# Kernel tuning notes

Measured on AMD Instinct MI355X. Metric: run time of the kernel, lower is better.

## Reference

```python
import jax, jax.numpy as jnp
import numpy as np

N_NODES = 50000
N_EDGES = 600000
NODE_DIM = 128
BOND_DIM = 16
HIDDEN = 128
DEPTH = 3


def setup_inputs() -> dict:
    key = jax.random.key(0)
    ks = jax.random.split(key, 10)
    rng = np.random.default_rng(0)
    half = N_EDGES // 2
    u = rng.integers(0, N_NODES, size=half)
    v = rng.integers(0, N_NODES, size=half)
    # forward edges followed by their reverses so rev_edge_index is well-defined
    edge_index = np.stack([np.concatenate([u, v]), np.concatenate([v, u])]).astype(np.int32)
    rev_edge_index = np.concatenate([np.arange(half, 2 * half), np.arange(0, half)]).astype(np.int32)

    def lin(k, fan_in, fan_out):
        kw, kb = jax.random.split(k)
        s = 1.0 / np.sqrt(fan_in)
        W = jax.random.uniform(kw, (fan_in, fan_out), jnp.float32, -s, s)
        b = jax.random.uniform(kb, (fan_out,), jnp.float32, -s, s)
        return W, b

    Wi, bi = lin(ks[0], NODE_DIM + BOND_DIM, HIDDEN)
    Wh, bh = lin(ks[1], HIDDEN, HIDDEN)
    Wo, bo = lin(ks[2], NODE_DIM + HIDDEN, HIDDEN)
    x = jax.random.normal(ks[3], (N_NODES, NODE_DIM), jnp.float32)
    edge_attr = jax.random.normal(ks[4], (N_EDGES, BOND_DIM), jnp.float32)
    return {
        "x": x,
        "edge_attr": edge_attr,
        "Wi": Wi, "bi": bi,
        "Wh": Wh, "bh": bh,
        "Wo": Wo, "bo": bo,
        "edge_index": jnp.asarray(edge_index),
        "rev_edge_index": jnp.asarray(rev_edge_index),
    }


def reference(x, edge_attr, Wi, bi, Wh, bh, Wo, bo, edge_index, rev_edge_index):
    # BondMessagePassing.forward (depth=3, dropout in eval mode = identity)
    src, dst = edge_index[0], edge_index[1]
    N = x.shape[0]
    # H_0 = relu(W_i([x[src] ; edge_attr]))  -> [E, H]
    H0 = jax.nn.relu(jnp.concatenate([x[src], edge_attr], axis=1) @ Wi + bi)
    H = H0
    for _ in range(DEPTH - 1):
        # aggregate incoming edge messages per node, then gather back to edges
        agg = jax.ops.segment_sum(H, dst, num_segments=N)  # [N, H]
        M = agg[src] - H[rev_edge_index]                   # subtract reverse-edge message
        H = jax.nn.relu(H0 + M @ Wh + bh)
    M = jax.ops.segment_sum(H, dst, num_segments=N)        # [N, H]
    # nodes with no incoming message fall back to their input features
    M = jnp.where(jnp.sum(M, axis=1, keepdims=True) == 0, x, M)
    return jax.nn.relu(jnp.concatenate([x, M], axis=1) @ Wo + bo)
```

## Files before the change

### kernel.cpp

```cpp
#include <hip/hip_runtime.h>
#include <hip/hip_bf16.h>

#define E_EDGES 600000
#define N_NODES 50000

typedef __attribute__((ext_vector_type(8))) short bf16x8;
typedef __attribute__((ext_vector_type(4))) short s16x4;
typedef __attribute__((ext_vector_type(4))) float f32x4;
typedef unsigned short u16;

static __device__ __forceinline__ float bf2f(u16 u) {
    unsigned int x = ((unsigned int)u) << 16;
    return __builtin_bit_cast(float, x);
}
static __device__ __forceinline__ u16 f2bf(float f) {
    return __builtin_bit_cast(u16, __float2bfloat16(f));
}
static __device__ __forceinline__ int xcd_swz(int orig, int nwg) {
    int q = nwg >> 3, r = nwg & 7;
    int x = orig & 7, o = orig >> 3;
    int base = (x < r) ? x * (q + 1) : r * (q + 1) + (x - r) * q;
    return base + o;
}

__global__ __launch_bounds__(256) void zero_kernel(f32x4* __restrict__ p, int n4) {
    int i = blockIdx.x * 256 + threadIdx.x;
    if (i < n4) p[i] = f32x4{0.f, 0.f, 0.f, 0.f};
}
__global__ __launch_bounds__(256) void zero_int_kernel(int* __restrict__ p, int n) {
    int i = blockIdx.x * 256 + threadIdx.x;
    if (i < n) p[i] = 0;
}

__global__ void prep_kernel(const float* __restrict__ Wi, const float* __restrict__ Wh,
                            const float* __restrict__ Wo,
                            short* __restrict__ WiT, short* __restrict__ WhT,
                            short* __restrict__ WoT) {
    int idx = blockIdx.x * 256 + threadIdx.x;
    if (idx < 128 * 160) {
        int j = idx / 160, k = idx % 160;
        WiT[idx] = (k < 144) ? (short)f2bf(Wi[k * 128 + j]) : (short)0;
    } else if (idx < 128 * 160 + 128 * 128) {
        int t = idx - 128 * 160;
        int j = t / 128, k = t % 128;
        WhT[t] = (short)f2bf(Wh[k * 128 + j]);
    } else if (idx < 128 * 160 + 128 * 128 + 128 * 256) {
        int t = idx - 128 * 160 - 128 * 128;
        int j = t / 256, k = t % 256;
        WoT[t] = (short)f2bf(Wo[k * 128 + j]);
    }
}

__global__ __launch_bounds__(256) void prepx_kernel(const float* __restrict__ x,
                                                    const float* __restrict__ ea,
                                                    short* __restrict__ xb,
                                                    short* __restrict__ eb) {
    const int NX4 = N_NODES * 128 / 4;
    const int NE4 = E_EDGES * 16 / 4;
    int i = blockIdx.x * 256 + threadIdx.x;
    if (i < NX4) {
        f32x4 v = ((const f32x4*)x)[i];
        s16x4 o;
#pragma unroll
        for (int j = 0; j < 4; ++j) o[j] = (short)f2bf(v[j]);
        ((s16x4*)xb)[i] = o;
    } else if (i < NX4 + NE4) {
        int t = i - NX4;
        f32x4 v = ((const f32x4*)ea)[t];
        s16x4 o;
#pragma unroll
        for (int j = 0; j < 4; ++j) o[j] = (short)f2bf(v[j]);
        ((s16x4*)eb)[t] = o;
    }
}

__global__ __launch_bounds__(256) void count_kernel(const int* __restrict__ ei,
                                                    int* __restrict__ deg) {
    int e = blockIdx.x * 256 + threadIdx.x;
    if (e < E_EDGES) atomicAdd(&deg[ei[E_EDGES + e]], 1);
}

__global__ __launch_bounds__(1024) void scan_kernel(const int* __restrict__ deg,
                                                    int* __restrict__ offs) {
    __shared__ int wsum[16];
    __shared__ int carry;
    const int t = threadIdx.x, lane = t & 63, wv = t >> 6;
    if (t == 0) { carry = 0; offs[0] = 0; }
    __syncthreads();
    for (int base = 0; base < N_NODES; base += 1024) {
        int i = base + t;
        int v = (i < N_NODES) ? deg[i] : 0;
        int s = v;
#pragma unroll
        for (int o = 1; o < 64; o <<= 1) {
            int u = __shfl_up(s, o, 64);
            if (lane >= o) s += u;
        }
        if (lane == 63) wsum[wv] = s;
        __syncthreads();
        if (wv == 0 && lane < 16) {
            int ws = wsum[lane];
#pragma unroll
            for (int o = 1; o < 16; o <<= 1) {
                int u = __shfl_up(ws, o, 16);
                if (lane >= o) ws += u;
            }
            wsum[lane] = ws;
        }
        __syncthreads();
        int wpre = (wv > 0) ? wsum[wv - 1] : 0;
        int incl = carry + wpre + s;
        if (i < N_NODES) offs[i + 1] = incl;
        __syncthreads();
        if (t == 1023) carry = incl;
        __syncthreads();
    }
}

__global__ __launch_bounds__(256) void scatter_kernel(const int* __restrict__ ei,
                                                      int* __restrict__ offs,
                                                      int* __restrict__ eids) {
    int e = blockIdx.x * 256 + threadIdx.x;
    if (e < E_EDGES) {
        int d = ei[E_EDGES + e];
        int p = atomicAdd(&offs[d], 1);
        eids[p] = e;
    }
}

__global__ __launch_bounds__(256) void segsum_kernel(const short* __restrict__ H,
                                                     const int* __restrict__ eids,
                                                     const int* __restrict__ offs,
                                                     float* __restrict__ agg,
                                                     float* __restrict__ flg) {
    const int w = threadIdx.x >> 6, l = threadIdx.x & 63;
    const int n = blockIdx.x * 4 + w;
    if (n >= N_NODES) return;
    int b = (n == 0) ? 0 : offs[n - 1];
    int en = offs[n];
    float s0 = 0.f, s1 = 0.f, t0 = 0.f, t1 = 0.f;
    int j = b;
    for (; j + 2 <= en; j += 2) {
        int e0 = eids[j], e1 = eids[j + 1];
        unsigned int pk0 = *(const unsigned int*)(H + (size_t)e0 * 128 + l * 2);
        unsigned int pk1 = *(const unsigned int*)(H + (size_t)e1 * 128 + l * 2);
        s0 += bf2f((u16)(pk0 & 0xffffu));
        s1 += bf2f((u16)(pk0 >> 16));
        t0 += bf2f((u16)(pk1 & 0xffffu));
        t1 += bf2f((u16)(pk1 >> 16));
    }
    if (j < en) {
        int e0 = eids[j];
        unsigned int pk0 = *(const unsigned int*)(H + (size_t)e0 * 128 + l * 2);
        s0 += bf2f((u16)(pk0 & 0xffffu));
        s1 += bf2f((u16)(pk0 >> 16));
    }
    s0 += t0; s1 += t1;
    agg[(size_t)n * 128 + l * 2] = s0;
    agg[(size_t)n * 128 + l * 2 + 1] = s1;
    if (flg) {
        float s = s0 + s1;
#pragma unroll
        for (int off = 32; off; off >>= 1) s += __shfl_xor(s, off, 64);
        if (l == 0) flg[n] = s;
    }
}

__global__ __launch_bounds__(256) void flag_kernel(const float* __restrict__ agg,
                                                   float* __restrict__ flg) {
    const int w = threadIdx.x >> 6, l = threadIdx.x & 63;
    const int n = blockIdx.x * 4 + w;
    if (n >= N_NODES) return;
    const float* r = agg + (size_t)n * 128 + l * 2;
    float s = r[0] + r[1];
#pragma unroll
    for (int off = 32; off; off >>= 1) s += __shfl_xor(s, off, 64);
    if (l == 0) flg[n] = s;
}

__global__ __launch_bounds__(256) void h0dst_kernel(
    const short* __restrict__ xb, const short* __restrict__ eb,
    const short* __restrict__ WiT, const float* __restrict__ bi,
    const int* __restrict__ ei, const int* __restrict__ eids,
    const int* __restrict__ offs, short* __restrict__ H0,
    float* __restrict__ agg1) {
    __shared__ short Bx[128 * 128];
    __shared__ short T[64 * 128];
    __shared__ int eloc[64], dstv[64];
    const int P = xcd_swz(blockIdx.x, gridDim.x) * 64;
    for (int i = threadIdx.x; i < 128 * 16; i += 256) {
        int row = i >> 4, cc = i & 15;
        int dstByte = row * 256 + ((cc * 16) ^ ((row & 7) << 4));
        *(bf16x8*)((char*)Bx + dstByte) = *(const bf16x8*)&WiT[row * 160 + cc * 8];
    }
    if (threadIdx.x < 64) {
        int e = eids[P + threadIdx.x];
        eloc[threadIdx.x] = e;
        dstv[threadIdx.x] = ei[E_EDGES + e];
    }
    __syncthreads();
    const int w = threadIdx.x >> 6, l = threadIdx.x & 63;
    const int c = l & 15, g = l >> 4;
    const int em = eloc[w * 16 + c];
    const int src_e = ei[em];
    const short* xr = xb + (size_t)src_e * 128;
    const short* ar = eb + (size_t)em * 16;

    bf16x8 px[4];
#pragma unroll
    for (int s = 0; s < 4; ++s) px[s] = *(const bf16x8*)(xr + s * 32 + g * 8);
    bf16x8 pe = {0, 0, 0, 0, 0, 0, 0, 0};
    if (g < 2) pe = *(const bf16x8*)(ar + g * 8);
    const int weOff = 128 + (g & 1) * 8;

    f32x4 acc[8] = {};
#pragma unroll
    for (int s = 0; s < 5; ++s) {
        const int k0 = s * 32 + g * 8;
        bf16x8 af = (s < 4) ? px[s] : pe;
#pragma unroll
        for (int nf = 0; nf < 8; ++nf) {
            const int row = nf * 16 + c;
            bf16x8 bfv;
            if (s < 4) {
                int bo = row * 256 + ((k0 * 2) ^ ((row & 7) << 4));
                bfv = *(const bf16x8*)((char*)Bx + bo);
            } else {
                bfv = *(const bf16x8*)&WiT[row * 160 + weOff];
            }
            acc[nf] = __builtin_amdgcn_mfma_f32_16x16x32_bf16(af, bfv, acc[nf], 0, 0, 0);
        }
    }
#pragma unroll
    for (int nf = 0; nf < 8; ++nf) {
        const int col = nf * 16 + c;
        const float bias = bi[col];
#pragma unroll
        for (int r = 0; r < 4; ++r) {
            const int lr2 = w * 16 + g * 4 + r;
            float v = fmaxf(acc[nf][r] + bias, 0.0f);
            int bo = lr2 * 256 + ((col * 2) ^ ((lr2 & 7) << 4));
            *(short*)((char*)T + bo) = (short)f2bf(v);
        }
    }
    __syncthreads();
#pragma unroll
    for (int it = 0; it < 4; ++it) {
        int i = threadIdx.x + it * 256;
        int lr = i >> 4, cc = i & 15;
        int bo = lr * 256 + ((cc * 16) ^ ((lr & 7) << 4));
        *(bf16x8*)&H0[(size_t)eloc[lr] * 128 + cc * 8] = *(const bf16x8*)((char*)T + bo);
    }
    {
        const int h = threadIdx.x >> 7;
        const int col = threadIdx.x & 127;
        const int base = h * 32;
        const int Ph = P + base;
        int n0 = dstv[base];
        bool fh0 = (((n0 == 0) ? 0 : offs[n0 - 1]) == Ph);
        bool fh1 = (offs[dstv[base + 31]] == Ph + 32);
        float sum = 0.f;
        int cur = n0, segStart = base;
        for (int lr = base; lr < base + 32; ++lr) {
            int d = dstv[lr];
            int bo = lr * 256 + ((col * 2) ^ ((lr & 7) << 4));
            float v = bf2f(*(const u16*)((char*)T + bo));
            if (d != cur) {
                bool comp = (segStart > base) || fh0;
                float* dp = agg1 + (size_t)cur * 128 + col;
                if (comp) *dp = sum; else atomicAdd(dp, sum);
                cur = d; segStart = lr; sum = v;
            } else {
                sum += v;
            }
        }
        bool comp = ((segStart > base) || fh0) && fh1;
        float* dp = agg1 + (size_t)cur * 128 + col;
        if (comp) *dp = sum; else atomicAdd(dp, sum);
    }
}

__global__ __launch_bounds__(256) void iter_dst_kernel(
    const float* __restrict__ agg1, const short* __restrict__ H0,
    const short* __restrict__ WhT, const float* __restrict__ bh,
    const int* __restrict__ ei, const int* __restrict__ rev,
    const int* __restrict__ eids, const int* __restrict__ offs,
    float* __restrict__ agg2) {
    __shared__ short B[128 * 136];
    __shared__ short T[64 * 136];
    __shared__ int eloc[64], dstv[64];
    const int P = xcd_swz(blockIdx.x, gridDim.x) * 64;
    for (int i = threadIdx.x; i < 128 * 16; i += 256) {
        int row = i >> 4, cc = i & 15;
        *(bf16x8*)&B[row * 136 + cc * 8] = *(const bf16x8*)&WhT[row * 128 + cc * 8];
    }
    if (threadIdx.x < 64) {
        int e = eids[P + threadIdx.x];
        eloc[threadIdx.x] = e;
        dstv[threadIdx.x] = ei[E_EDGES + e];
    }
    __syncthreads();
    const int w = threadIdx.x >> 6, l = threadIdx.x & 63;
    const int c = l & 15, g = l >> 4;
    const int e_m = eloc[w * 16 + c];
    const int src_e = ei[e_m];
    const int rev_e = rev[e_m];
    const float* arow = agg1 + (size_t)src_e * 128;
    const short* hrow = H0 + (size_t)rev_e * 128;

    bf16x8 stg[4];
#pragma unroll
    for (int it = 0; it < 4; ++it) {
        int i = threadIdx.x + it * 256;
        int lr = i >> 4, cc = i & 15;
        stg[it] = *(const bf16x8*)&H0[(size_t)eloc[lr] * 128 + cc * 8];
    }
    f32x4 pa[4][2];
    bf16x8 ph[4];
#pragma unroll
    for (int s = 0; s < 4; ++s) {
        pa[s][0] = *(const f32x4*)(arow + s * 32 + g * 8);
        pa[s][1] = *(const f32x4*)(arow + s * 32 + g * 8 + 4);
        ph[s] = *(const bf16x8*)(hrow + s * 32 + g * 8);
    }
#pragma unroll
    for (int it = 0; it < 4; ++it) {
        int i = threadIdx.x + it * 256;
        int lr = i >> 4, cc = i & 15;
        *(bf16x8*)&T[lr * 136 + cc * 8] = stg[it];
    }
    __syncthreads();

    f32x4 acc[8] = {};
#pragma unroll
    for (int s = 0; s < 4; ++s) {
        const int k0 = s * 32 + g * 8;
        bf16x8 af;
#pragma unroll
        for (int j = 0; j < 8; ++j) {
            float aj = ((j < 4) ? pa[s][0][j] : pa[s][1][j - 4]) - bf2f((u16)ph[s][j]);
            af[j] = (short)f2bf(aj);
        }
#pragma unroll
        for (int nf = 0; nf < 8; ++nf) {
            bf16x8 bfv = *(const bf16x8*)&B[(nf * 16 + c) * 136 + k0];
            acc[nf] = __builtin_amdgcn_mfma_f32_16x16x32_bf16(af, bfv, acc[nf], 0, 0, 0);
        }
    }
#pragma unroll
    for (int nf = 0; nf < 8; ++nf) {
        const int col = nf * 16 + c;
        const float bias = bh[col];
#pragma unroll
        for (int r = 0; r < 4; ++r) {
            const int lr2 = w * 16 + g * 4 + r;
            float res = bf2f((u16)T[lr2 * 136 + col]);
            float v = fmaxf(acc[nf][r] + bias + res, 0.0f);
            T[lr2 * 136 + col] = (short)f2bf(v);
        }
    }
    __syncthreads();
    {
        const int h = threadIdx.x >> 7;
        const int col = threadIdx.x & 127;
        const int base = h * 32;
        const int Ph = P + base;
        int n0 = dstv[base];
        bool fh0 = (((n0 == 0) ? 0 : offs[n0 - 1]) == Ph);
        bool fh1 = (offs[dstv[base + 31]] == Ph + 32);
        float sum = 0.f;
        int cur = n0, segStart = base;
        for (int lr = base; lr < base + 32; ++lr) {
            int d = dstv[lr];
            float v = bf2f((u16)T[lr * 136 + col]);
            if (d != cur) {
                bool comp = (segStart > base) || fh0;
                float* dp = agg2 + (size_t)cur * 128 + col;
                if (comp) *dp = sum; else atomicAdd(dp, sum);
                cur = d; segStart = lr; sum = v;
            } else {
                sum += v;
            }
        }
        bool comp = ((segStart > base) || fh0) && fh1;
        float* dp = agg2 + (size_t)cur * 128 + col;
        if (comp) *dp = sum; else atomicAdd(dp, sum);
    }
}

__global__ __launch_bounds__(256) void iter2F_kernel(
    const float* __restrict__ agg1, const float* __restrict__ agg2,
    const short* __restrict__ H0, const short* __restrict__ WhT,
    const float* __restrict__ bh, const int* __restrict__ ei,
    const int* __restrict__ rev, const int* __restrict__ eids,
    const int* __restrict__ offs, float* __restrict__ aggF) {
    __shared__ short B[128 * 128];
    __shared__ short TR[64 * 128];
    __shared__ int eloc[64], dstv[64], revl[64];
    const int P = xcd_swz(blockIdx.x, gridDim.x) * 64;
    for (int i = threadIdx.x; i < 128 * 16; i += 256) {
        int row = i >> 4, cc = i & 15;
        int dstByte = row * 256 + ((cc * 16) ^ ((row & 7) << 4));
        *(bf16x8*)((char*)B + dstByte) = *(const bf16x8*)&WhT[row * 128 + cc * 8];
    }
    if (threadIdx.x < 64) {
        int e = eids[P + threadIdx.x];
        eloc[threadIdx.x] = e;
        dstv[threadIdx.x] = ei[E_EDGES + e];
        revl[threadIdx.x] = rev[e];
    }
    __syncthreads();
#pragma unroll
    for (int it = 0; it < 4; ++it) {
        int i = threadIdx.x + it * 256;
        int lr = i >> 4, cc = i & 15;
        int bo = lr * 256 + ((cc * 16) ^ ((lr & 7) << 4));
        *(bf16x8*)((char*)TR + bo) = *(const bf16x8*)&H0[(size_t)revl[lr] * 128 + cc * 8];
    }
    const int w = threadIdx.x >> 6, l = threadIdx.x & 63;
    const int c = l & 15, g = l >> 4;
    const int rl = w * 16 + c;
    const int em = eloc[rl];
    const int dst_em = dstv[rl];
    const int src_m = ei[em];
    const short* h0row = H0 + (size_t)em * 128;
    const float* a1row = agg1 + (size_t)dst_em * 128;
    const float* a2row = agg2 + (size_t)src_m * 128;

    bf16x8 ph[4];
    f32x4 pa1[4][2], pa2[4][2];
#pragma unroll
    for (int s = 0; s < 4; ++s) {
        ph[s] = *(const bf16x8*)(h0row + s * 32 + g * 8);
        pa1[s][0] = *(const f32x4*)(a1row + s * 32 + g * 8);
        pa1[s][1] = *(const f32x4*)(a1row + s * 32 + g * 8 + 4);
        pa2[s][0] = *(const f32x4*)(a2row + s * 32 + g * 8);
        pa2[s][1] = *(const f32x4*)(a2row + s * 32 + g * 8 + 4);
    }
    __syncthreads();

    f32x4 acc[8] = {};
#pragma unroll
    for (int s = 0; s < 4; ++s) {
        const int k0 = s * 32 + g * 8;
        bf16x8 af;
#pragma unroll
        for (int j = 0; j < 8; ++j) {
            float aj = ((j < 4) ? pa1[s][0][j] : pa1[s][1][j - 4]) - bf2f((u16)ph[s][j]);
            af[j] = (short)f2bf(aj);
        }
#pragma unroll
        for (int nf = 0; nf < 8; ++nf) {
            const int row = nf * 16 + c;
            int bo = row * 256 + ((k0 * 2) ^ ((row & 7) << 4));
            bf16x8 bfv = *(const bf16x8*)((char*)B + bo);
            acc[nf] = __builtin_amdgcn_mfma_f32_16x16x32_bf16(af, bfv, acc[nf], 0, 0, 0);
        }
    }
#pragma unroll
    for (int nf = 0; nf < 8; ++nf) {
        const int col = nf * 16 + c;
        const float bias = bh[col];
#pragma unroll
        for (int r = 0; r < 4; ++r) {
            const int lr2 = w * 16 + g * 4 + r;
            int bo = lr2 * 256 + ((col * 2) ^ ((lr2 & 7) << 4));
            float res = bf2f(*(const u16*)((char*)TR + bo));
            float v = fmaxf(acc[nf][r] + bias + res, 0.0f);
            *(short*)((char*)TR + bo) = (short)f2bf(v);
        }
    }
    __syncthreads();
    f32x4 acc2[8] = {};
#pragma unroll
    for (int s = 0; s < 4; ++s) {
        const int k0 = s * 32 + g * 8;
        int boT = rl * 256 + ((k0 * 2) ^ ((rl & 7) << 4));
        bf16x8 hv = *(const bf16x8*)((char*)TR + boT);
        bf16x8 af;
#pragma unroll
        for (int j = 0; j < 8; ++j) {
            float aj = ((j < 4) ? pa2[s][0][j] : pa2[s][1][j - 4]) - bf2f((u16)hv[j]);
            af[j] = (short)f2bf(aj);
        }
#pragma unroll
        for (int nf = 0; nf < 8; ++nf) {
            const int row = nf * 16 + c;
            int bo = row * 256 + ((k0 * 2) ^ ((row & 7) << 4));
            bf16x8 bfv = *(const bf16x8*)((char*)B + bo);
            acc2[nf] = __builtin_amdgcn_mfma_f32_16x16x32_bf16(af, bfv, acc2[nf], 0, 0, 0);
        }
    }
    __syncthreads();
#pragma unroll
    for (int nf = 0; nf < 8; ++nf) {
        const int col = nf * 16 + c;
        const float bias = bh[col];
#pragma unroll
        for (int r = 0; r < 4; ++r) {
            const int lr2 = w * 16 + g * 4 + r;
            float res = bf2f((u16)H0[(size_t)eloc[lr2] * 128 + col]);
            float v = fmaxf(acc2[nf][r] + bias + res, 0.0f);
            int bo = lr2 * 256 + ((col * 2) ^ ((lr2 & 7) << 4));
            *(short*)((char*)TR + bo) = (short)f2bf(v);
        }
    }
    __syncthreads();
    {
        const int h = threadIdx.x >> 7;
        const int col = threadIdx.x & 127;
        const int base = h * 32;
        const int Ph = P + base;
        int n0 = dstv[base];
        bool fh0 = (((n0 == 0) ? 0 : offs[n0 - 1]) == Ph);
        bool fh1 = (offs[dstv[base + 31]] == Ph + 32);
        float sum = 0.f;
        int cur = n0, segStart = base;
        for (int lr = base; lr < base + 32; ++lr) {
            int d = dstv[lr];
            int bo = lr * 256 + ((col * 2) ^ ((lr & 7) << 4));
            float v = bf2f(*(const u16*)((char*)TR + bo));
            if (d != cur) {
                bool comp = (segStart > base) || fh0;
                float* dp = aggF + (size_t)cur * 128 + col;
                if (comp) *dp = sum; else atomicAdd(dp, sum);
                cur = d; segStart = lr; sum = v;
            } else {
                sum += v;
            }
        }
        bool comp = ((segStart > base) || fh0) && fh1;
        float* dp = aggF + (size_t)cur * 128 + col;
        if (comp) *dp = sum; else atomicAdd(dp, sum);
    }
}

__global__ __launch_bounds__(256) void h0s_kernel(
    const float* __restrict__ x, const float* __restrict__ eattr,
    const short* __restrict__ WiT, const float* __restrict__ bi,
    const int* __restrict__ ei, short* __restrict__ H0) {
    __shared__ short B[128 * 168];
    for (int i = threadIdx.x; i < 128 * 20; i += 256) {
        int row = i / 20, cc = i % 20;
        *(bf16x8*)&B[row * 168 + cc * 8] = *(const bf16x8*)&WiT[row * 160 + cc * 8];
    }
    __syncthreads();
    const int w = threadIdx.x >> 6, l = threadIdx.x & 63;
    const int c = l & 15, g = l >> 4;
    const int e0 = blockIdx.x * 64 + w * 16;
    const int em = e0 + c;
    const int src_e = ei[em];
    const float* xr = x + (size_t)src_e * 128;
    const float* ar = eattr + (size_t)em * 16;

    f32x4 acc[8] = {};
#pragma unroll
    for (int s = 0; s < 5; ++s) {
        const int k0 = s * 32 + g * 8;
        float av[8];
        if (s < 4) {
            f32x4 p0 = *(const f32x4*)(xr + k0);
            f32x4 p1 = *(const f32x4*)(xr + k0 + 4);
#pragma unroll
            for (int j = 0; j < 4; ++j) { av[j] = p0[j]; av[j + 4] = p1[j]; }
        } else {
            if (g < 2) {
                f32x4 p0 = *(const f32x4*)(ar + g * 8);
                f32x4 p1 = *(const f32x4*)(ar + g * 8 + 4);
#pragma unroll
                for (int j = 0; j < 4; ++j) { av[j] = p0[j]; av[j + 4] = p1[j]; }
            } else {
#pragma unroll
                for (int j = 0; j < 8; ++j) av[j] = 0.f;
            }
        }
        bf16x8 af;
#pragma unroll
        for (int j = 0; j < 8; ++j) af[j] = (short)f2bf(av[j]);
#pragma unroll
        for (int nf = 0; nf < 8; ++nf) {
            bf16x8 bfv = *(const bf16x8*)&B[(nf * 16 + c) * 168 + k0];
            acc[nf] = __builtin_amdgcn_mfma_f32_16x16x32_bf16(af, bfv, acc[nf], 0, 0, 0);
        }
    }
#pragma unroll
    for (int nf = 0; nf < 8; ++nf) {
        const int col = nf * 16 + c;
        const float bias = bi[col];
#pragma unroll
        for (int r = 0; r < 4; ++r) {
            const int er = e0 + g * 4 + r;
            float v = fmaxf(acc[nf][r] + bias, 0.0f);
            H0[(size_t)er * 128 + col] = (short)f2bf(v);
        }
    }
}

__global__ __launch_bounds__(256) void iterx_kernel(
    const float* __restrict__ agg, const short* __restrict__ Hrev,
    const short* Hres, const short* __restrict__ WhT,
    const float* __restrict__ bh, const int* __restrict__ ei,
    const int* __restrict__ rev, short* Hout) {
    __shared__ short B[128 * 136];
    for (int i = threadIdx.x; i < 128 * 16; i += 256) {
        int row = i >> 4, cc = i & 15;
        *(bf16x8*)&B[row * 136 + cc * 8] = *(const bf16x8*)&WhT[row * 128 + cc * 8];
    }
    __syncthreads();
    const int w = threadIdx.x >> 6, l = threadIdx.x & 63;
    const int c = l & 15, g = l >> 4;
    const int e0 = blockIdx.x * 64 + w * 16;
    const int em = e0 + c;
    const int src_e = ei[em];
    const int rev_e = rev[em];
    const float* arow = agg + (size_t)src_e * 128;
    const short* hrow = Hrev + (size_t)rev_e * 128;

    f32x4 acc[8] = {};
#pragma unroll
    for (int s = 0; s < 4; ++s) {
        const int k0 = s * 32 + g * 8;
        f32x4 p0 = *(const f32x4*)(arow + k0);
        f32x4 p1 = *(const f32x4*)(arow + k0 + 4);
        bf16x8 hv = *(const bf16x8*)(hrow + k0);
        bf16x8 af;
#pragma unroll
        for (int j = 0; j < 8; ++j) {
            float aj = ((j < 4) ? p0[j] : p1[j - 4]) - bf2f((u16)hv[j]);
            af[j] = (short)f2bf(aj);
        }
#pragma unroll
        for (int nf = 0; nf < 8; ++nf) {
            bf16x8 bfv = *(const bf16x8*)&B[(nf * 16 + c) * 136 + k0];
            acc[nf] = __builtin_amdgcn_mfma_f32_16x16x32_bf16(af, bfv, acc[nf], 0, 0, 0);
        }
    }
#pragma unroll
    for (int nf = 0; nf < 8; ++nf) {
        const int col = nf * 16 + c;
        const float bias = bh[col];
#pragma unroll
        for (int r = 0; r < 4; ++r) {
            const int er = e0 + g * 4 + r;
            float v = acc[nf][r] + bias + bf2f((u16)Hres[(size_t)er * 128 + col]);
            v = fmaxf(v, 0.0f);
            Hout[(size_t)er * 128 + col] = (short)f2bf(v);
        }
    }
}

__global__ __launch_bounds__(256) void h0_kernel(
    const float* __restrict__ x, const float* __restrict__ eattr,
    const short* __restrict__ WiT, const float* __restrict__ bi,
    const int* __restrict__ ei, short* __restrict__ H0, float* __restrict__ agg) {
    __shared__ short B[128 * 168];
    for (int i = threadIdx.x; i < 128 * 20; i += 256) {
        int row = i / 20, cc = i % 20;
        *(bf16x8*)&B[row * 168 + cc * 8] = *(const bf16x8*)&WiT[row * 160 + cc * 8];
    }
    __syncthreads();
    const int w = threadIdx.x >> 6, l = threadIdx.x & 63;
    const int c = l & 15, g = l >> 4;
    const int e0 = blockIdx.x * 64 + w * 16;
    const int em = e0 + c;
    const int src_e = ei[em];
    const float* xr = x + (size_t)src_e * 128;
    const float* ar = eattr + (size_t)em * 16;
    f32x4 acc[8] = {};
#pragma unroll
    for (int s = 0; s < 5; ++s) {
        const int k0 = s * 32 + g * 8;
        float av[8];
        if (s < 4) {
            f32x4 p0 = *(const f32x4*)(xr + k0);
            f32x4 p1 = *(const f32x4*)(xr + k0 + 4);
#pragma unroll
            for (int j = 0; j < 4; ++j) { av[j] = p0[j]; av[j + 4] = p1[j]; }
        } else {
            if (g < 2) {
                f32x4 p0 = *(const f32x4*)(ar + g * 8);
                f32x4 p1 = *(const f32x4*)(ar + g * 8 + 4);
#pragma unroll
                for (int j = 0; j < 4; ++j) { av[j] = p0[j]; av[j + 4] = p1[j]; }
            } else {
#pragma unroll
                for (int j = 0; j < 8; ++j) av[j] = 0.f;
            }
        }
        bf16x8 af;
#pragma unroll
        for (int j = 0; j < 8; ++j) af[j] = (short)f2bf(av[j]);
#pragma unroll
        for (int nf = 0; nf < 8; ++nf) {
            bf16x8 bfv = *(const bf16x8*)&B[(nf * 16 + c) * 168 + k0];
            acc[nf] = __builtin_amdgcn_mfma_f32_16x16x32_bf16(af, bfv, acc[nf], 0, 0, 0);
        }
    }
    int dsts[4];
#pragma unroll
    for (int r = 0; r < 4; ++r) dsts[r] = ei[E_EDGES + e0 + g * 4 + r];
#pragma unroll
    for (int nf = 0; nf < 8; ++nf) {
        const int col = nf * 16 + c;
        const float bias = bi[col];
#pragma unroll
        for (int r = 0; r < 4; ++r) {
            const int er = e0 + g * 4 + r;
            float v = fmaxf(acc[nf][r] + bias, 0.0f);
            u16 hb = f2bf(v);
            H0[(size_t)er * 128 + col] = (short)hb;
            atomicAdd(agg + (size_t)dsts[r] * 128 + col, bf2f(hb));
        }
    }
}

__global__ __launch_bounds__(256) void iter_atomic_kernel(
    const float* __restrict__ aggin, const short* __restrict__ Hin,
    const short* __restrict__ H0, const short* __restrict__ WhT,
    const float* __restrict__ bh, const int* __restrict__ ei,
    const int* __restrict__ rev, float* __restrict__ aggout) {
    __shared__ short B[128 * 136];
    for (int i = threadIdx.x; i < 128 * 16; i += 256) {
        int row = i >> 4, cc = i & 15;
        *(bf16x8*)&B[row * 136 + cc * 8] = *(const bf16x8*)&WhT[row * 128 + cc * 8];
    }
    __syncthreads();
    const int w = threadIdx.x >> 6, l = threadIdx.x & 63;
    const int c = l & 15, g = l >> 4;
    const int e0 = blockIdx.x * 64 + w * 16;
    const int em = e0 + c;
    const int src_e = ei[em];
    const int rev_e = rev[em];
    const float* arow = aggin + (size_t)src_e * 128;
    const short* hrow = Hin + (size_t)rev_e * 128;

    f32x4 acc[8] = {};
#pragma unroll
    for (int s = 0; s < 4; ++s) {
        const int k0 = s * 32 + g * 8;
        f32x4 p0 = *(const f32x4*)(arow + k0);
        f32x4 p1 = *(const f32x4*)(arow + k0 + 4);
        bf16x8 hv = *(const bf16x8*)(hrow + k0);
        bf16x8 af;
#pragma unroll
        for (int j = 0; j < 8; ++j) {
            float aj = ((j < 4) ? p0[j] : p1[j - 4]) - bf2f((u16)hv[j]);
            af[j] = (short)f2bf(aj);
        }
#pragma unroll
        for (int nf = 0; nf < 8; ++nf) {
            bf16x8 bfv = *(const bf16x8*)&B[(nf * 16 + c) * 136 + k0];
            acc[nf] = __builtin_amdgcn_mfma_f32_16x16x32_bf16(af, bfv, acc[nf], 0, 0, 0);
        }
    }
    int dsts[4];
#pragma unroll
    for (int r = 0; r < 4; ++r) dsts[r] = ei[E_EDGES + e0 + g * 4 + r];
#pragma unroll
    for (int nf = 0; nf < 8; ++nf) {
        const int col = nf * 16 + c;
        const float bias = bh[col];
#pragma unroll
        for (int r = 0; r < 4; ++r) {
            const int er = e0 + g * 4 + r;
            float v = acc[nf][r] + bias + bf2f((u16)H0[(size_t)er * 128 + col]);
            v = fmaxf(v, 0.0f);
            atomicAdd(aggout + (size_t)dsts[r] * 128 + col, bf2f(f2bf(v)));
        }
    }
}

__global__ __launch_bounds__(256) void iter2c_kernel(
    const float* __restrict__ agg1, const float* __restrict__ agg2,
    const short* __restrict__ H0, const short* __restrict__ WhT,
    const float* __restrict__ bh, const int* __restrict__ ei,
    const int* __restrict__ rev, float* __restrict__ aggF) {
    __shared__ short B[128 * 136];
    __shared__ short T[4][16 * 136];
    for (int i = threadIdx.x; i < 128 * 16; i += 256) {
        int row = i >> 4, cc = i & 15;
        *(bf16x8*)&B[row * 136 + cc * 8] = *(const bf16x8*)&WhT[row * 128 + cc * 8];
    }
    __syncthreads();
    const int w = threadIdx.x >> 6, l = threadIdx.x & 63;
    const int c = l & 15, g = l >> 4;
    const int e0 = blockIdx.x * 64 + w * 16;
    const int em = e0 + c;
    const int dst_em = ei[E_EDGES + em];
    const int src_em = ei[em];
    const float* a1row = agg1 + (size_t)dst_em * 128;
    const float* a2row = agg2 + (size_t)src_em * 128;
    const short* h0row = H0 + (size_t)em * 128;
    int rows[4], revs[4], dsts[4];
#pragma unroll
    for (int r = 0; r < 4; ++r) {
        rows[r] = e0 + g * 4 + r;
        revs[r] = rev[rows[r]];
        dsts[r] = ei[E_EDGES + rows[r]];
    }
    f32x4 acc[8] = {};
#pragma unroll
    for (int s = 0; s < 4; ++s) {
        const int k0 = s * 32 + g * 8;
        f32x4 p0 = *(const f32x4*)(a1row + k0);
        f32x4 p1 = *(const f32x4*)(a1row + k0 + 4);
        bf16x8 hv = *(const bf16x8*)(h0row + k0);
        bf16x8 af;
#pragma unroll
        for (int j = 0; j < 8; ++j) {
            float aj = ((j < 4) ? p0[j] : p1[j - 4]) - bf2f((u16)hv[j]);
            af[j] = (short)f2bf(aj);
        }
#pragma unroll
        for (int nf = 0; nf < 8; ++nf) {
            bf16x8 bfv = *(const bf16x8*)&B[(nf * 16 + c) * 136 + k0];
            acc[nf] = __builtin_amdgcn_mfma_f32_16x16x32_bf16(af, bfv, acc[nf], 0, 0, 0);
        }
    }
#pragma unroll
    for (int nf = 0; nf < 8; ++nf) {
        const int col = nf * 16 + c;
        const float bias = bh[col];
#pragma unroll
        for (int r = 0; r < 4; ++r) {
            float res = bf2f((u16)H0[(size_t)revs[r] * 128 + col]);
            float v = fmaxf(acc[nf][r] + bias + res, 0.0f);
            T[w][(g * 4 + r) * 136 + col] = (short)f2bf(v);
        }
    }
    __syncthreads();
    f32x4 acc2[8] = {};
#pragma unroll
    for (int s = 0; s < 4; ++s) {
        const int k0 = s * 32 + g * 8;
        f32x4 p0 = *(const f32x4*)(a2row + k0);
        f32x4 p1 = *(const f32x4*)(a2row + k0 + 4);
        bf16x8 hv = *(const bf16x8*)&T[w][c * 136 + k0];
        bf16x8 af;
#pragma unroll
        for (int j = 0; j < 8; ++j) {
            float aj = ((j < 4) ? p0[j] : p1[j - 4]) - bf2f((u16)hv[j]);
            af[j] = (short)f2bf(aj);
        }
#pragma unroll
        for (int nf = 0; nf < 8; ++nf) {
            bf16x8 bfv = *(const bf16x8*)&B[(nf * 16 + c) * 136 + k0];
            acc2[nf] = __builtin_amdgcn_mfma_f32_16x16x32_bf16(af, bfv, acc2[nf], 0, 0, 0);
        }
    }
#pragma unroll
    for (int nf = 0; nf < 8; ++nf) {
        const int col = nf * 16 + c;
        const float bias = bh[col];
#pragma unroll
        for (int r = 0; r < 4; ++r) {
            float res = bf2f((u16)H0[(size_t)rows[r] * 128 + col]);
            float v = fmaxf(acc2[nf][r] + bias + res, 0.0f);
            atomicAdd(aggF + (size_t)dsts[r] * 128 + col, v);
        }
    }
}

__global__ __launch_bounds__(256) void out_kernel(
    const float* __restrict__ x, const float* agg,
    const float* __restrict__ flg, const short* __restrict__ WoT,
    const float* __restrict__ bo, float* out) {
    __shared__ short B[128 * 256];
    for (int i = threadIdx.x; i < 128 * 32; i += 256) {
        int row = i >> 5, cc = i & 31;
        int dstByte = row * 512 + ((cc * 16) ^ ((row & 7) << 4));
        *(bf16x8*)((char*)B + dstByte) = *(const bf16x8*)&WoT[row * 256 + cc * 8];
    }
    __syncthreads();
    const int w = threadIdx.x >> 6, l = threadIdx.x & 63;
    const int c = l & 15, g = l >> 4;
    const int n0 = blockIdx.x * 64 + w * 16;
    const int nm = n0 + c;
    const int nmc = nm < N_NODES ? nm : N_NODES - 1;
    const float* xr = x + (size_t)nmc * 128;
    const float* mr = agg + (size_t)nmc * 128;
    const bool usex = (flg[nmc] == 0.0f);
    f32x4 acc[8] = {};
#pragma unroll
    for (int s = 0; s < 8; ++s) {
        const int k0 = s * 32 + g * 8;
        const float* srcp;
        int kk;
        if (s < 4) { srcp = xr; kk = k0; }
        else       { srcp = usex ? xr : mr; kk = k0 - 128; }
        f32x4 p0 = *(const f32x4*)(srcp + kk);
        f32x4 p1 = *(const f32x4*)(srcp + kk + 4);
        bf16x8 af;
#pragma unroll
        for (int j = 0; j < 4; ++j) {
            af[j] = (short)f2bf(p0[j]);
            af[j + 4] = (short)f2bf(p1[j]);
        }
#pragma unroll
        for (int nf = 0; nf < 8; ++nf) {
            int row = nf * 16 + c;
            int byteOff = row * 512 + ((k0 * 2) ^ ((row & 7) << 4));
            bf16x8 bfv = *(const bf16x8*)((char*)B + byteOff);
            acc[nf] = __builtin_amdgcn_mfma_f32_16x16x32_bf16(af, bfv, acc[nf], 0, 0, 0);
        }
    }
#pragma unroll
    for (int nf = 0; nf < 8; ++nf) {
        const int col = nf * 16 + c;
        const float bias = bo[col];
#pragma unroll
        for (int r = 0; r < 4; ++r) {
            const int er = n0 + g * 4 + r;
            if (er < N_NODES) {
                float v = fmaxf(acc[nf][r] + bias, 0.0f);
                out[(size_t)er * 128 + col] = v;
            }
        }
    }
}

extern "C" void kernel_launch(void* const* d_in, const int* in_sizes, int n_in,
                              void* d_out, int out_size, void* d_ws, size_t ws_size,
                              hipStream_t stream) {
    const float* x     = (const float*)d_in[0];
    const float* eattr = (const float*)d_in[1];
    const float* Wi    = (const float*)d_in[2];
    const float* bi    = (const float*)d_in[3];
    const float* Wh    = (const float*)d_in[4];
    const float* bh    = (const float*)d_in[5];
    const float* Wo    = (const float*)d_in[6];
    const float* bo    = (const float*)d_in[7];
    const int*   ei    = (const int*)d_in[8];
    const int*   rev   = (const int*)d_in[9];
    float* out = (float*)d_out;
    (void)in_sizes; (void)n_in; (void)out_size;

    char* ws = (char*)d_ws;
    size_t off = 0;
    auto alloc = [&](size_t bytes) {
        void* p = ws + off;
        off = (off + bytes + 255) & ~(size_t)255;
        return p;
    };
    const int AGG4 = N_NODES * 128 / 4;
    const int EG = E_EDGES / 64;
    const int EB = (E_EDGES + 255) / 256;
    const int NB4 = (N_NODES + 3) / 4;
    const int PREPG = (128 * 160 + 128 * 128 + 128 * 256 + 255) / 256;
    const int PREPXG = (N_NODES * 128 / 4 + E_EDGES * 16 / 4 + 255) / 256;

    if (ws_size >= (size_t)337 * 1000 * 1000) {
        short* H0  = (short*)alloc((size_t)E_EDGES * 128 * 2);
        short* H1  = (short*)alloc((size_t)E_EDGES * 128 * 2);
        float* agg = (float*)alloc((size_t)N_NODES * 128 * 4);
        float* flg = (float*)alloc((size_t)N_NODES * 4);
        short* WiT = (short*)alloc(128 * 160 * 2);
        short* WhT = (short*)alloc(128 * 128 * 2);
        short* WoT = (short*)alloc(128 * 256 * 2);
        int* deg   = (int*)alloc((size_t)N_NODES * 4);
        int* offs  = (int*)alloc((size_t)(N_NODES + 1) * 4);
        int* eids  = (int*)alloc((size_t)E_EDGES * 4);

        zero_int_kernel<<<(N_NODES + 255) / 256, 256, 0, stream>>>(deg, N_NODES);
        prep_kernel<<<PREPG, 256, 0, stream>>>(Wi, Wh, Wo, WiT, WhT, WoT);
        count_kernel<<<EB, 256, 0, stream>>>(ei, deg);
        scan_kernel<<<1, 1024, 0, stream>>>(deg, offs);
        scatter_kernel<<<EB, 256, 0, stream>>>(ei, offs, eids);
        h0s_kernel<<<EG, 256, 0, stream>>>(x, eattr, WiT, bi, ei, H0);
        segsum_kernel<<<NB4, 256, 0, stream>>>(H0, eids, offs, agg, nullptr);
        iterx_kernel<<<EG, 256, 0, stream>>>(agg, H0, H0, WhT, bh, ei, rev, H1);
        segsum_kernel<<<NB4, 256, 0, stream>>>(H1, eids, offs, agg, nullptr);
        iterx_kernel<<<EG, 256, 0, stream>>>(agg, H1, H0, WhT, bh, ei, rev, H0);
        segsum_kernel<<<NB4, 256, 0, stream>>>(H0, eids, offs, out, flg);
        out_kernel<<<(N_NODES + 63) / 64, 256, 0, stream>>>(x, out, flg, WoT, bo, out);
    } else if (ws_size >= (size_t)210 * 1000 * 1000) {
        short* H0   = (short*)alloc((size_t)E_EDGES * 128 * 2);
        float* agg1 = (float*)alloc((size_t)N_NODES * 128 * 4);
        float* agg2 = (float*)alloc((size_t)N_NODES * 128 * 4);
        float* flg  = (float*)alloc((size_t)N_NODES * 4);
        short* WiT  = (short*)alloc(128 * 160 * 2);
        short* WhT  = (short*)alloc(128 * 128 * 2);
        short* WoT  = (short*)alloc(128 * 256 * 2);
        int* deg    = (int*)alloc((size_t)N_NODES * 4);
        int* offs   = (int*)alloc((size_t)(N_NODES + 1) * 4);
        int* eids   = (int*)alloc((size_t)E_EDGES * 4);
        short* xbuf = (short*)agg2;
        short* ebuf = (short*)out;

        zero_int_kernel<<<(N_NODES + 255) / 256, 256, 0, stream>>>(deg, N_NODES);
        zero_kernel<<<(AGG4 + 255) / 256, 256, 0, stream>>>((f32x4*)agg1, AGG4);
        prep_kernel<<<PREPG, 256, 0, stream>>>(Wi, Wh, Wo, WiT, WhT, WoT);
        prepx_kernel<<<PREPXG, 256, 0, stream>>>(x, eattr, xbuf, ebuf);
        count_kernel<<<EB, 256, 0, stream>>>(ei, deg);
        scan_kernel<<<1, 1024, 0, stream>>>(deg, offs);
        scatter_kernel<<<EB, 256, 0, stream>>>(ei, offs, eids);
        h0dst_kernel<<<EG, 256, 0, stream>>>(xbuf, ebuf, WiT, bi, ei, eids, offs, H0, agg1);
        zero_kernel<<<(AGG4 + 255) / 256, 256, 0, stream>>>((f32x4*)agg2, AGG4);
        zero_kernel<<<(AGG4 + 255) / 256, 256, 0, stream>>>((f32x4*)out, AGG4);
        iter_dst_kernel<<<EG, 256, 0, stream>>>(agg1, H0, WhT, bh, ei, rev, eids, offs, agg2);
        iter2F_kernel<<<EG, 256, 0, stream>>>(agg1, agg2, H0, WhT, bh, ei, rev, eids, offs, out);
        flag_kernel<<<NB4, 256, 0, stream>>>(out, flg);
        out_kernel<<<(N_NODES + 63) / 64, 256, 0, stream>>>(x, out, flg, WoT, bo, out);
    } else {
        short* H0   = (short*)alloc((size_t)E_EDGES * 128 * 2);
        float* agg1 = (float*)alloc((size_t)N_NODES * 128 * 4);
        float* agg2 = (float*)alloc((size_t)N_NODES * 128 * 4);
        float* flg  = (float*)alloc((size_t)N_NODES * 4);
        short* WiT  = (short*)alloc(128 * 160 * 2);
        short* WhT  = (short*)alloc(128 * 128 * 2);
        short* WoT  = (short*)alloc(128 * 256 * 2);
        float* aggF = out;

        zero_kernel<<<(AGG4 + 255) / 256, 256, 0, stream>>>((f32x4*)agg1, AGG4);
        zero_kernel<<<(AGG4 + 255) / 256, 256, 0, stream>>>((f32x4*)agg2, AGG4);
        zero_kernel<<<(AGG4 + 255) / 256, 256, 0, stream>>>((f32x4*)aggF, AGG4);
        prep_kernel<<<PREPG, 256, 0, stream>>>(Wi, Wh, Wo, WiT, WhT, WoT);
        h0_kernel<<<EG, 256, 0, stream>>>(x, eattr, WiT, bi, ei, H0, agg1);
        iter_atomic_kernel<<<EG, 256, 0, stream>>>(agg1, H0, H0, WhT, bh, ei, rev, agg2);
        iter2c_kernel<<<EG, 256, 0, stream>>>(agg1, agg2, H0, WhT, bh, ei, rev, aggF);
        flag_kernel<<<NB4, 256, 0, stream>>>(aggF, flg);
        out_kernel<<<(N_NODES + 63) / 64, 256, 0, stream>>>(x, aggF, flg, WoT, bo, out);
    }
}
```

Before: 613.4 us.

## Store H0 in destination-sorted order and precompute reverse-edge positions

H0 rows are now written at their sorted position (P+lr) rather than at the original edge id. Own-row reads in the later kernels therefore become contiguous instead of scattered. Two new kernels build a pos_of inverse permutation and a posrev table, so reverse-edge gathers index the permuted H0 directly. Buffers are also aliased (deg and pos_of inside H0, flg inside agg1) to stay within the workspace, at the cost of two extra small passes.

```diff
diff --git a/kernel.cpp b/kernel.cpp
--- a/kernel.cpp
+++ b/kernel.cpp
@@ -126,6 +126,19 @@
         int p = atomicAdd(&offs[d], 1);
         eids[p] = e;
     }
+}
+
+__global__ __launch_bounds__(256) void posA_kernel(const int* __restrict__ eids,
+                                                   int* __restrict__ pos_of) {
+    int p = blockIdx.x * 256 + threadIdx.x;
+    if (p < E_EDGES) pos_of[eids[p]] = p;
+}
+__global__ __launch_bounds__(256) void posB_kernel(const int* __restrict__ eids,
+                                                   const int* __restrict__ rev,
+                                                   const int* __restrict__ pos_of,
+                                                   int* __restrict__ posrev) {
+    int p = blockIdx.x * 256 + threadIdx.x;
+    if (p < E_EDGES) posrev[p] = pos_of[rev[eids[p]]];
 }
 
 __global__ __launch_bounds__(256) void segsum_kernel(const short* __restrict__ H,
@@ -249,7 +262,7 @@
         int i = threadIdx.x + it * 256;
         int lr = i >> 4, cc = i & 15;
         int bo = lr * 256 + ((cc * 16) ^ ((lr & 7) << 4));
-        *(bf16x8*)&H0[(size_t)eloc[lr] * 128 + cc * 8] = *(const bf16x8*)((char*)T + bo);
+        *(bf16x8*)&H0[(size_t)(P + lr) * 128 + cc * 8] = *(const bf16x8*)((char*)T + bo);
     }
     {
         const int h = threadIdx.x >> 7;
@@ -283,7 +296,7 @@
 __global__ __launch_bounds__(256) void iter_dst_kernel(
     const float* __restrict__ agg1, const short* __restrict__ H0,
     const short* __restrict__ WhT, const float* __restrict__ bh,
-    const int* __restrict__ ei, const int* __restrict__ rev,
+    const int* __restrict__ ei, const int* __restrict__ posrev,
     const int* __restrict__ eids, const int* __restrict__ offs,
     float* __restrict__ agg2) {
     __shared__ short B[128 * 136];
@@ -302,18 +315,17 @@
     __syncthreads();
     const int w = threadIdx.x >> 6, l = threadIdx.x & 63;
     const int c = l & 15, g = l >> 4;
-    const int e_m = eloc[w * 16 + c];
-    const int src_e = ei[e_m];
-    const int rev_e = rev[e_m];
+    const int src_e = ei[eloc[w * 16 + c]];
+    const int prv = posrev[P + w * 16 + c];
     const float* arow = agg1 + (size_t)src_e * 128;
-    const short* hrow = H0 + (size_t)rev_e * 128;
+    const short* hrow = H0 + (size_t)prv * 128;
 
     bf16x8 stg[4];
 #pragma unroll
     for (int it = 0; it < 4; ++it) {
         int i = threadIdx.x + it * 256;
         int lr = i >> 4, cc = i & 15;
-        stg[it] = *(const bf16x8*)&H0[(size_t)eloc[lr] * 128 + cc * 8];
+        stg[it] = *(const bf16x8*)&H0[(size_t)(P + lr) * 128 + cc * 8];
     }
     f32x4 pa[4][2];
     bf16x8 ph[4];
@@ -392,11 +404,11 @@
     const float* __restrict__ agg1, const float* __restrict__ agg2,
     const short* __restrict__ H0, const short* __restrict__ WhT,
     const float* __restrict__ bh, const int* __restrict__ ei,
-    const int* __restrict__ rev, const int* __restrict__ eids,
+    const int* __restrict__ posrev, const int* __restrict__ eids,
     const int* __restrict__ offs, float* __restrict__ aggF) {
     __shared__ short B[128 * 128];
     __shared__ short TR[64 * 128];
-    __shared__ int eloc[64], dstv[64], revl[64];
+    __shared__ int eloc[64], dstv[64], prl[64];
     const int P = xcd_swz(blockIdx.x, gridDim.x) * 64;
     for (int i = threadIdx.x; i < 128 * 16; i += 256) {
         int row = i >> 4, cc = i & 15;
@@ -407,7 +419,7 @@
         int e = eids[P + threadIdx.x];
         eloc[threadIdx.x] = e;
         dstv[threadIdx.x] = ei[E_EDGES + e];
-        revl[threadIdx.x] = rev[e];
+        prl[threadIdx.x] = posrev[P + threadIdx.x];
     }
     __syncthreads();
 #pragma unroll
@@ -415,7 +427,7 @@
         int i = threadIdx.x + it * 256;
         int lr = i >> 4, cc = i & 15;
         int bo = lr * 256 + ((cc * 16) ^ ((lr & 7) << 4));
-        *(bf16x8*)((char*)TR + bo) = *(const bf16x8*)&H0[(size_t)revl[lr] * 128 + cc * 8];
+        *(bf16x8*)((char*)TR + bo) = *(const bf16x8*)&H0[(size_t)prl[lr] * 128 + cc * 8];
     }
     const int w = threadIdx.x >> 6, l = threadIdx.x & 63;
     const int c = l & 15, g = l >> 4;
@@ -423,7 +435,7 @@
     const int em = eloc[rl];
     const int dst_em = dstv[rl];
     const int src_m = ei[em];
-    const short* h0row = H0 + (size_t)em * 128;
+    const short* h0row = H0 + (size_t)(P + rl) * 128;
     const float* a1row = agg1 + (size_t)dst_em * 128;
     const float* a2row = agg2 + (size_t)src_m * 128;
 
@@ -499,7 +511,7 @@
 #pragma unroll
         for (int r = 0; r < 4; ++r) {
             const int lr2 = w * 16 + g * 4 + r;
-            float res = bf2f((u16)H0[(size_t)eloc[lr2] * 128 + col]);
+            float res = bf2f((u16)H0[(size_t)(P + lr2) * 128 + col]);
             float v = fmaxf(acc2[nf][r] + bias + res, 0.0f);
             int bo = lr2 * 256 + ((col * 2) ^ ((lr2 & 7) << 4));
             *(short*)((char*)TR + bo) = (short)f2bf(v);
@@ -974,18 +986,20 @@
         segsum_kernel<<<NB4, 256, 0, stream>>>(H0, eids, offs, out, flg);
         out_kernel<<<(N_NODES + 63) / 64, 256, 0, stream>>>(x, out, flg, WoT, bo, out);
     } else if (ws_size >= (size_t)210 * 1000 * 1000) {
-        short* H0   = (short*)alloc((size_t)E_EDGES * 128 * 2);
-        float* agg1 = (float*)alloc((size_t)N_NODES * 128 * 4);
-        float* agg2 = (float*)alloc((size_t)N_NODES * 128 * 4);
-        float* flg  = (float*)alloc((size_t)N_NODES * 4);
-        short* WiT  = (short*)alloc(128 * 160 * 2);
-        short* WhT  = (short*)alloc(128 * 128 * 2);
-        short* WoT  = (short*)alloc(128 * 256 * 2);
-        int* deg    = (int*)alloc((size_t)N_NODES * 4);
-        int* offs   = (int*)alloc((size_t)(N_NODES + 1) * 4);
-        int* eids   = (int*)alloc((size_t)E_EDGES * 4);
-        short* xbuf = (short*)agg2;
-        short* ebuf = (short*)out;
+        short* H0     = (short*)alloc((size_t)E_EDGES * 128 * 2);
+        float* agg1   = (float*)alloc((size_t)N_NODES * 128 * 4);
+        float* agg2   = (float*)alloc((size_t)N_NODES * 128 * 4);
+        short* WiT    = (short*)alloc(128 * 160 * 2);
+        short* WhT    = (short*)alloc(128 * 128 * 2);
+        short* WoT    = (short*)alloc(128 * 256 * 2);
+        int* offs     = (int*)alloc((size_t)(N_NODES + 1) * 4);
+        int* eids     = (int*)alloc((size_t)E_EDGES * 4);
+        int* posrev   = (int*)alloc((size_t)E_EDGES * 4);
+        float* flg    = (float*)agg1;
+        int* deg      = (int*)H0;
+        int* pos_of   = (int*)((char*)H0 + 4 * 1024 * 1024);
+        short* xbuf   = (short*)agg2;
+        short* ebuf   = (short*)out;
 
         zero_int_kernel<<<(N_NODES + 255) / 256, 256, 0, stream>>>(deg, N_NODES);
         zero_kernel<<<(AGG4 + 255) / 256, 256, 0, stream>>>((f32x4*)agg1, AGG4);
@@ -994,11 +1008,13 @@
         count_kernel<<<EB, 256, 0, stream>>>(ei, deg);
         scan_kernel<<<1, 1024, 0, stream>>>(deg, offs);
         scatter_kernel<<<EB, 256, 0, stream>>>(ei, offs, eids);
+        posA_kernel<<<EB, 256, 0, stream>>>(eids, pos_of);
+        posB_kernel<<<EB, 256, 0, stream>>>(eids, rev, pos_of, posrev);
         h0dst_kernel<<<EG, 256, 0, stream>>>(xbuf, ebuf, WiT, bi, ei, eids, offs, H0, agg1);
         zero_kernel<<<(AGG4 + 255) / 256, 256, 0, stream>>>((f32x4*)agg2, AGG4);
         zero_kernel<<<(AGG4 + 255) / 256, 256, 0, stream>>>((f32x4*)out, AGG4);
-        iter_dst_kernel<<<EG, 256, 0, stream>>>(agg1, H0, WhT, bh, ei, rev, eids, offs, agg2);
-        iter2F_kernel<<<EG, 256, 0, stream>>>(agg1, agg2, H0, WhT, bh, ei, rev, eids, offs, out);
+        iter_dst_kernel<<<EG, 256, 0, stream>>>(agg1, H0, WhT, bh, ei, posrev, eids, offs, agg2);
+        iter2F_kernel<<<EG, 256, 0, stream>>>(agg1, agg2, H0, WhT, bh, ei, posrev, eids, offs, out);
         flag_kernel<<<NB4, 256, 0, stream>>>(out, flg);
         out_kernel<<<(N_NODES + 63) / 64, 256, 0, stream>>>(x, out, flg, WoT, bo, out);
     } else {
```

New measurement: 610.0 us. About the same (-0.6%).
